# Performance work log

Measured on AMD Instinct MI355X. Metric: run time of the kernel, lower is better.

The kernel has to match this reference:

```python
import jax, jax.numpy as jnp
import numpy as np

D, H = 1536, 16
HD = D // H            # head_dim = 96
ROPE_CH = HD // 2      # rope_channels_ratio=0.5 -> RoPE on last 48 channels
FF = 4 * D             # SwiGLU hidden
EPS = 1e-6
MAX_WAVELENGTH = 10000.0


def _ln(x):
    # LayerNorm, elementwise_affine=False, eps=1e-6
    m = jnp.mean(x, axis=-1, keepdims=True)
    v = jnp.var(x, axis=-1, keepdims=True)
    return (x - m) * jax.lax.rsqrt(v + EPS)


def _rms(x, w):
    # LlamaRMSNorm: fp32 internally
    xf = x.astype(jnp.float32)
    v = jnp.mean(jnp.square(xf), axis=-1, keepdims=True)
    return (w * (xf * jax.lax.rsqrt(v + EPS))).astype(x.dtype)


def _apply_rope(q, pos):
    # q: [B,H,S,hd], pos: [B,S]
    hd = q.shape[-1]
    frac = 2.0 * jnp.arange(hd // 2, dtype=jnp.float32) / hd
    timescale = MAX_WAVELENGTH ** frac                       # [hd/2]
    sin_inp = pos.astype(jnp.float32)[:, None, :, None] / timescale  # [B,1,S,hd/2]
    sin, cos = jnp.sin(sin_inp), jnp.cos(sin_inp)
    a, b = jnp.split(q, 2, axis=-1)
    out = jnp.concatenate([a * cos - b * sin, b * cos + a * sin], axis=-1)
    return out.astype(q.dtype)


def _rotary(x, pos, ch):
    # apply RoPE to the last `ch` channels of head_dim
    left, right = x[..., :-ch], x[..., -ch:]
    return jnp.concatenate([left, _apply_rope(right, pos)], axis=-1)


def _mod(x, shift, scale):
    # t2i_modulate: x * (1 + scale) + shift, cond broadcast over seq
    return x * (1.0 + scale[:, None, :]) + shift[:, None, :]


def setup_inputs() -> dict:
    key = jax.random.key(0)
    ks = jax.random.split(key, 32)
    B, Nx, Ny = 1, 2048, 256
    w = lambda k, shp: (0.02 * jax.random.normal(k, shp, dtype=jnp.float32))
    inp = {
        'x': jax.random.normal(ks[0], (B, Nx, D), dtype=jnp.float32),
        'y': jax.random.normal(ks[1], (B, Ny, D), dtype=jnp.float32),
        't': jax.random.normal(ks[2], (B, D), dtype=jnp.float32),
        'positions': jnp.arange(Nx, dtype=jnp.int32).reshape(B, Nx),
        'w_mod_x': w(ks[3], (D, 6 * D)), 'b_mod_x': jnp.zeros((6 * D,), jnp.float32),
        'w_mod_y': w(ks[4], (D, 6 * D)), 'b_mod_y': jnp.zeros((6 * D,), jnp.float32),
        'w_qkv_x': w(ks[5], (D, 3 * D)), 'b_qkv_x': jnp.zeros((3 * D,), jnp.float32),
        'w_qkv_y': w(ks[6], (D, 3 * D)), 'b_qkv_y': jnp.zeros((3 * D,), jnp.float32),
        'qn_x': jnp.ones((HD,), jnp.float32), 'kn_x': jnp.ones((HD,), jnp.float32),
        'qn_y': jnp.ones((HD,), jnp.float32), 'kn_y': jnp.ones((HD,), jnp.float32),
        'w_proj_x': w(ks[7], (D, D)), 'b_proj_x': jnp.zeros((D,), jnp.float32),
        'w_proj_y': w(ks[8], (D, D)), 'b_proj_y': jnp.zeros((D,), jnp.float32),
        'w1_x': w(ks[9], (D, FF)), 'w2_x': w(ks[10], (D, FF)), 'w3_x': w(ks[11], (FF, D)),
        'w1_y': w(ks[12], (D, FF)), 'w2_y': w(ks[13], (D, FF)), 'w3_y': w(ks[14], (FF, D)),
    }
    return inp


def reference(x, y, t, positions,
              w_mod_x, b_mod_x, w_mod_y, b_mod_y,
              w_qkv_x, b_qkv_x, w_qkv_y, b_qkv_y,
              qn_x, kn_x, qn_y, kn_y,
              w_proj_x, b_proj_x, w_proj_y, b_proj_y,
              w1_x, w2_x, w3_x, w1_y, w2_y, w3_y):
    B, Nx, _ = x.shape
    Ny = y.shape[1]
    st = jax.nn.silu(t)
    sh1x, sc1x, g1x, sh2x, sc2x, g2x = jnp.split(st @ w_mod_x + b_mod_x, 6, axis=-1)
    sh1y, sc1y, g1y, sh2y, sc2y, g2y = jnp.split(st @ w_mod_y + b_mod_y, 6, axis=-1)

    def qkv(z, w, b, qn, kn, pos):
        q, k, v = jnp.split(z @ w + b, 3, axis=-1)
        r = lambda u: u.reshape(B, -1, H, HD).transpose(0, 2, 1, 3)  # [B,H,S,hd]
        q, k, v = r(q), r(k), r(v)
        q, k = _rms(q, qn), _rms(k, kn)
        if pos is not None:
            q, k = _rotary(q, pos, ROPE_CH), _rotary(k, pos, ROPE_CH)
        return q, k, v

    qx, kx, vx = qkv(_mod(_ln(x), sh1x, sc1x), w_qkv_x, b_qkv_x, qn_x, kn_x, positions)
    qy, ky, vy = qkv(_mod(_ln(y), sh1y, sc1y), w_qkv_y, b_qkv_y, qn_y, kn_y, None)

    q = jnp.concatenate([qx, qy], axis=2)
    k = jnp.concatenate([kx, ky], axis=2)
    v = jnp.concatenate([vx, vy], axis=2)
    scores = jnp.einsum('bhqd,bhkd->bhqk', q, k) * (HD ** -0.5)
    attn = jax.nn.softmax(scores, axis=-1)
    o = jnp.einsum('bhqk,bhkd->bhqd', attn, v)
    o = o.transpose(0, 2, 1, 3).reshape(B, Nx + Ny, D)
    ox, oy = o[:, :Nx], o[:, Nx:]

    x = x + g1x[:, None, :] * (ox @ w_proj_x + b_proj_x)
    y = y + g1y[:, None, :] * (oy @ w_proj_y + b_proj_y)

    def ffn(z, w1, w2, w3):
        return (jax.nn.silu(z @ w1) * (z @ w2)) @ w3

    x = x + g2x[:, None, :] * ffn(_mod(_ln(x), sh2x, sc2x), w1_x, w2_x, w3_x)
    y = y + g2y[:, None, :] * ffn(_mod(_ln(y), sh2y, sc2y), w1_y, w2_y, w3_y)
    return jnp.concatenate([x, y], axis=1)
```

## Files before the change

### kernel.cpp

```cpp
#include <hip/hip_runtime.h>
#include <hip/hip_bf16.h>

#define D_  1536
#define H_  16
#define HD_ 96
#define NX_ 2048
#define NY_ 256
#define NT_ 2304
#define FF_ 6144
#define EPS_ 1e-6f

typedef unsigned short u16;
typedef unsigned int   u32;
typedef short short8 __attribute__((ext_vector_type(8)));
typedef float f32x4  __attribute__((ext_vector_type(4)));
typedef unsigned short u16x4 __attribute__((ext_vector_type(4)));

__device__ __forceinline__ u16 f2bf(float f){
    u32 u = __float_as_uint(f);
    return (u16)((u + 0x7fffu + ((u >> 16) & 1u)) >> 16);
}
__device__ __forceinline__ float bf2f(u16 h){ return __uint_as_float(((u32)h) << 16); }

__device__ __forceinline__ void gll16(const void* g, void* l){
    __builtin_amdgcn_global_load_lds(
        (const __attribute__((address_space(1))) unsigned int*)g,
        (__attribute__((address_space(3))) unsigned int*)l, 16, 0, 0);
}

__global__ __launch_bounds__(256) void transpose_k(
    const float* __restrict__ Wx, const float* __restrict__ Wy,
    u16* __restrict__ Ox, u16* __restrict__ Oy, int K, int N)
{
    const float* W = blockIdx.y ? Wy : Wx;
    u16* O = blockIdx.y ? Oy : Ox;
    int tn_cnt = N >> 5;
    int tk = blockIdx.x / tn_cnt, tn = blockIdx.x % tn_cnt;
    __shared__ float tile[32][33];
    int t = threadIdx.x;
    {
        int k = t >> 3, n4 = (t & 7) * 4;
        float4 v = *(const float4*)&W[(size_t)(tk*32 + k) * N + tn*32 + n4];
        tile[k][n4+0] = v.x; tile[k][n4+1] = v.y;
        tile[k][n4+2] = v.z; tile[k][n4+3] = v.w;
    }
    __syncthreads();
    {
        int n = t >> 3, k4 = (t & 7) * 4;
        u16x4 r;
        #pragma unroll
        for (int i = 0; i < 4; i++) r[i] = f2bf(tile[k4+i][n]);
        *(u16x4*)&O[(size_t)(tn*32 + n) * K + tk*32 + k4] = r;
    }
}

__global__ __launch_bounds__(256) void modvec2_k(
    const float* __restrict__ t_in,
    const float* __restrict__ w_mod_x, const float* __restrict__ w_mod_y,
    float* __restrict__ pbuf)
{
    int part = blockIdx.y;
    int j = blockIdx.x * 256 + threadIdx.x;
    __shared__ float st[96];
    int k0 = part * 96;
    if (threadIdx.x < 96){
        float v = t_in[k0 + threadIdx.x];
        st[threadIdx.x] = v / (1.f + __expf(-v));
    }
    __syncthreads();
    const float* W; int col;
    if (j < 6*D_){ W = w_mod_x; col = j; }
    else         { W = w_mod_y; col = j - 6*D_; }
    const float* wp = W + (size_t)k0 * (6*D_) + col;
    float acc = 0.f;
    #pragma unroll 8
    for (int k = 0; k < 96; k++)
        acc += st[k] * wp[(size_t)k * (6*D_)];
    pbuf[(size_t)part * 18432 + j] = acc;
}

__global__ __launch_bounds__(256) void reducemod_k(
    const float* __restrict__ pbuf,
    const float* __restrict__ b_mod_x, const float* __restrict__ b_mod_y,
    float* __restrict__ modx, float* __restrict__ mody)
{
    int j = blockIdx.x * 256 + threadIdx.x;
    float acc = (j < 6*D_) ? b_mod_x[j] : b_mod_y[j - 6*D_];
    #pragma unroll
    for (int p = 0; p < 16; p++)
        acc += pbuf[(size_t)p * 18432 + j];
    if (j < 6*D_) modx[j] = acc;
    else          mody[j - 6*D_] = acc;
}

__global__ __launch_bounds__(256) void lnmod_k(
    const float* __restrict__ inx, const float* __restrict__ iny,
    const float* __restrict__ modx, const float* __restrict__ mody,
    int shoff, u16* __restrict__ out)
{
    int row = blockIdx.x, t = threadIdx.x;
    const float* in; const float* mod;
    if (row < NX_){ in = inx + (size_t)row * D_;        mod = modx; }
    else          { in = iny + (size_t)(row-NX_) * D_;  mod = mody; }
    const float* sh = mod + shoff;
    const float* sc = mod + shoff + D_;
    float vals[6]; float s = 0.f, ss = 0.f;
    #pragma unroll
    for (int j = 0; j < 6; j++){
        float v = in[t + j*256];
        vals[j] = v; s += v; ss += v*v;
    }
    for (int mask = 1; mask < 64; mask <<= 1){
        s  += __shfl_xor(s,  mask);
        ss += __shfl_xor(ss, mask);
    }
    __shared__ float red[2][4];
    int wave = t >> 6, lane = t & 63;
    if (lane == 0){ red[0][wave] = s; red[1][wave] = ss; }
    __syncthreads();
    s  = red[0][0] + red[0][1] + red[0][2] + red[0][3];
    ss = red[1][0] + red[1][1] + red[1][2] + red[1][3];
    float mean = s * (1.f / D_);
    float var  = ss * (1.f / D_) - mean * mean;
    float inv  = rsqrtf(var + EPS_);
    #pragma unroll
    for (int j = 0; j < 6; j++){
        int c = t + j*256;
        float z = (vals[j] - mean) * inv;
        z = z * (1.f + sc[c]) + sh[c];
        out[(size_t)row * D_ + c] = f2bf(z);
    }
}

template<int MODE>
__global__ __launch_bounds__(512, 2) void gemm3_k(
    const u16* __restrict__ A,
    const u16* __restrict__ BTx, const u16* __restrict__ BTy,
    const float* __restrict__ biasx, const float* __restrict__ biasy,
    const u16* __restrict__ hmul,
    u16* __restrict__ outB, int ldo,
    int K, int mb, int nb)
{
    __shared__ u16 As[2][256*64];
    __shared__ u16 Bs[2][256*64];
    int nwg = mb * nb;
    int bid = blockIdx.x;
    int q = nwg >> 3, r = nwg & 7, xcd = bid & 7;
    int wgid = (xcd < r ? xcd*(q+1) : r*(q+1) + (xcd - r)*q) + (bid >> 3);
    int bm = wgid % mb, bn = wgid / mb;
    int sel = (bm == mb - 1);
    int row0 = bm * 256, col0 = bn * 256;
    const u16* Bt = sel ? BTy : BTx;

    int t = threadIdx.x, wid = t >> 6, lane = t & 63;
    int lrow = lane & 15, lgrp = lane >> 4;
    int wr = (wid >> 2) * 128, wc = (wid & 3) * 64;

    const char* Ab = (const char*)(A  + (size_t)row0 * K);
    const char* Bb = (const char*)(Bt + (size_t)col0 * K);
    u32 offG[4], offL[4];
    #pragma unroll
    for (int i = 0; i < 4; i++){
        int rr = i*64 + (t >> 3);
        int cc = (t & 7) ^ (rr & 7);
        offG[i] = (u32)(rr * K + cc * 8) * 2;
        offL[i] = (u32)(i*8192 + t*16);
    }

    #define STAGEG(bsel, kb) do{                                                  \
        _Pragma("unroll")                                                         \
        for (int i = 0; i < 4; i++)                                               \
            gll16(Ab + (offG[i] + (kb)), (char*)As[bsel] + offL[i]);              \
        _Pragma("unroll")                                                         \
        for (int i = 0; i < 4; i++)                                               \
            gll16(Bb + (offG[i] + (kb)), (char*)Bs[bsel] + offL[i]);              \
    } while(0)

    f32x4 acc[8][4];
    #pragma unroll
    for (int i = 0; i < 8; i++)
        #pragma unroll
        for (int j = 0; j < 4; j++) acc[i][j] = (f32x4){0.f,0.f,0.f,0.f};

    int nt = K >> 6;
    STAGEG(0, 0);

    for (int tt = 0; tt < nt; tt++){
        const u16* Ac = As[tt & 1];
        const u16* Bc = Bs[tt & 1];
        if (tt + 1 < nt){
            STAGEG((tt + 1) & 1, (u32)(tt + 1) * 128);
            asm volatile("s_waitcnt vmcnt(8)" ::: "memory");
        } else {
            asm volatile("s_waitcnt vmcnt(0)" ::: "memory");
        }
        __builtin_amdgcn_sched_barrier(0);
        __builtin_amdgcn_s_barrier();
        __builtin_amdgcn_sched_barrier(0);
        #pragma unroll
        for (int kk = 0; kk < 2; kk++){
            int pc = ((kk*4 + lgrp) ^ (lrow & 7)) * 8;
            short8 bf[4];
            #pragma unroll
            for (int ni = 0; ni < 4; ni++)
                bf[ni] = *(const short8*)&Bc[(wc + ni*16 + lrow)*64 + pc];
            #pragma unroll
            for (int mi = 0; mi < 8; mi++){
                short8 af = *(const short8*)&Ac[(wr + mi*16 + lrow)*64 + pc];
                #pragma unroll
                for (int ni = 0; ni < 4; ni++)
                    acc[mi][ni] = __builtin_amdgcn_mfma_f32_16x16x32_bf16(
                                      af, bf[ni], acc[mi][ni], 0, 0, 0);
            }
        }
        asm volatile("s_waitcnt lgkmcnt(0)" ::: "memory");
        __builtin_amdgcn_sched_barrier(0);
        __builtin_amdgcn_s_barrier();
        __builtin_amdgcn_sched_barrier(0);
    }
    #undef STAGEG

    const float* biasp = sel ? biasy : biasx;
    #pragma unroll
    for (int mi = 0; mi < 8; mi++){
        #pragma unroll
        for (int ni = 0; ni < 4; ni++){
            #pragma unroll
            for (int rr = 0; rr < 4; rr++){
                int gr = row0 + wr + mi*16 + lgrp*4 + rr;
                int gc = col0 + wc + ni*16 + lrow;
                float v = acc[mi][ni][rr];
                size_t oi = (size_t)gr * ldo + gc;
                if (MODE == 0)      outB[oi] = f2bf(v + biasp[gc]);
                else if (MODE == 2) outB[oi] = f2bf(v / (1.f + __expf(-v)));
                else if (MODE == 3) outB[oi] = f2bf(bf2f(hmul[oi]) * v);
            }
        }
    }
}

template<int MODE>
__global__ __launch_bounds__(256, 2) void gemm2_k(
    const u16* __restrict__ A, int lda,
    const u16* __restrict__ BTx, const u16* __restrict__ BTy, int ldb,
    const float* __restrict__ biasx, const float* __restrict__ biasy,
    const float* __restrict__ residx, const float* __restrict__ residy,
    const float* __restrict__ gmodx, const float* __restrict__ gmody,
    float* __restrict__ outF, int ldo,
    int K, int nb, int kparts)
{
    __shared__ u16 As[2][128*64];
    __shared__ u16 Bs[2][128*64];
    int nwg_base = 18 * nb;
    int nwg = nwg_base * kparts;
    int bid = blockIdx.x;
    int bid2 = (bid & 7) * (nwg >> 3) + (bid >> 3);
    int ks  = bid2 / nwg_base;
    int rem = bid2 % nwg_base;
    int bm = rem % 18, bn = rem / 18;
    int sel = (bm >= 16);
    int row0 = bm * 128, col0 = bn * 128;
    const u16* Bt = (sel ? BTy : BTx) + (size_t)ks * K;
    const u16* Ap = A + (size_t)ks * K;
    outF += (size_t)ks * NT_ * D_;

    int t = threadIdx.x, w = t >> 6, l = t & 63;
    int lrow = l & 15, lgrp = l >> 4;
    int wr = (w >> 1) * 64, wc = (w & 1) * 64;

    const char* Ab = (const char*)(Ap + (size_t)row0 * lda);
    const char* Bb = (const char*)(Bt + (size_t)col0 * ldb);
    u32 offA[4], offB[4], ldsoff[4];
    #pragma unroll
    for (int i = 0; i < 4; i++){
        int r = (i*4 + w)*8 + (l >> 3);
        int c = (l & 7) ^ (r & 7);
        offA[i]   = (u32)(r * lda + c * 8) * 2;
        offB[i]   = (u32)(r * ldb + c * 8) * 2;
        ldsoff[i] = (u32)((i*4 + w) * 1024);
    }

    #define STAGEG(bsel, kb) do{                                                  \
        _Pragma("unroll")                                                         \
        for (int i = 0; i < 4; i++)                                               \
            gll16(Ab + (offA[i] + (kb)), (char*)As + (bsel)*16384 + ldsoff[i]);   \
        _Pragma("unroll")                                                         \
        for (int i = 0; i < 4; i++)                                               \
            gll16(Bb + (offB[i] + (kb)), (char*)Bs + (bsel)*16384 + ldsoff[i]);   \
    } while(0)

    f32x4 acc[4][4];
    #pragma unroll
    for (int i = 0; i < 4; i++)
        #pragma unroll
        for (int j = 0; j < 4; j++) acc[i][j] = (f32x4){0.f,0.f,0.f,0.f};

    int nt = K >> 6;
    STAGEG(0, 0);

    for (int tt = 0; tt < nt; tt++){
        const u16* Ac = As[tt & 1];
        const u16* Bc = Bs[tt & 1];
        if (tt + 1 < nt){
            STAGEG((tt + 1) & 1, (u32)(tt + 1) * 128);
            asm volatile("s_waitcnt vmcnt(8)" ::: "memory");
        } else {
            asm volatile("s_waitcnt vmcnt(0)" ::: "memory");
        }
        __builtin_amdgcn_sched_barrier(0);
        __builtin_amdgcn_s_barrier();
        __builtin_amdgcn_sched_barrier(0);
        #pragma unroll
        for (int kk = 0; kk < 2; kk++){
            int pc = ((kk*4 + lgrp) ^ (lrow & 7)) * 8;
            short8 af[4], bf[4];
            #pragma unroll
            for (int mi = 0; mi < 4; mi++)
                af[mi] = *(const short8*)&Ac[(wr + mi*16 + lrow)*64 + pc];
            #pragma unroll
            for (int ni = 0; ni < 4; ni++)
                bf[ni] = *(const short8*)&Bc[(wc + ni*16 + lrow)*64 + pc];
            #pragma unroll
            for (int mi = 0; mi < 4; mi++)
                #pragma unroll
                for (int ni = 0; ni < 4; ni++)
                    acc[mi][ni] = __builtin_amdgcn_mfma_f32_16x16x32_bf16(
                                      af[mi], bf[ni], acc[mi][ni], 0, 0, 0);
        }
        asm volatile("s_waitcnt lgkmcnt(0)" ::: "memory");
        __builtin_amdgcn_sched_barrier(0);
        __builtin_amdgcn_s_barrier();
        __builtin_amdgcn_sched_barrier(0);
    }
    #undef STAGEG

    const float* biasp  = sel ? biasy  : biasx;
    const float* residp = sel ? residy : residx;
    const float* gmodp  = sel ? gmody  : gmodx;
    #pragma unroll
    for (int mi = 0; mi < 4; mi++){
        #pragma unroll
        for (int ni = 0; ni < 4; ni++){
            #pragma unroll
            for (int r = 0; r < 4; r++){
                int gr = row0 + wr + mi*16 + lgrp*4 + r;
                int gc = col0 + wc + ni*16 + lrow;
                float v = acc[mi][ni][r];
                size_t oi = (size_t)gr * ldo + gc;
                if (MODE == 1)      outF[oi] = residp[oi] + gmodp[gc] * (v + biasp[gc]);
                else if (MODE == 5) outF[oi] = v;
            }
        }
    }
}

__global__ __launch_bounds__(256) void reduce_k(
    const float* __restrict__ p, const float* __restrict__ x1,
    const float* __restrict__ modx, const float* __restrict__ mody,
    float* __restrict__ dout)
{
    size_t i = ((size_t)blockIdx.x * 256 + threadIdx.x) * 4;
    float4 a = *(const float4*)&p[i];
    float4 b = *(const float4*)&p[(size_t)NT_ * D_ + i];
    float4 r = *(const float4*)&x1[i];
    int row = (int)(i / D_), col = (int)(i % D_);
    const float* g = (row < NX_ ? modx : mody) + 5*D_;
    float4 gv = *(const float4*)&g[col];
    float4 o;
    o.x = r.x + gv.x * (a.x + b.x);
    o.y = r.y + gv.y * (a.y + b.y);
    o.z = r.z + gv.z * (a.z + b.z);
    o.w = r.w + gv.w * (a.w + b.w);
    *(float4*)&dout[i] = o;
}

__global__ __launch_bounds__(256) void qkvpost_k(
    const u16* __restrict__ qkvraw, const int* __restrict__ positions,
    const float* __restrict__ qn_x, const float* __restrict__ kn_x,
    const float* __restrict__ qn_y, const float* __restrict__ kn_y,
    u16* __restrict__ Qg, u16* __restrict__ Kg, u16* __restrict__ Vg)
{
    int tok = blockIdx.x;
    int t = threadIdx.x, wave = t >> 6, lane = t & 63;
    bool isx = tok < NX_;
    float pos = isx ? (float)positions[tok] : 0.f;
    const float* qn = isx ? qn_x : qn_y;
    const float* kn = isx ? kn_x : kn_y;
    bool act = lane < 48;
    int d = lane * 2;
    #pragma unroll
    for (int hh = 0; hh < 4; hh++){
        int h = wave + hh * 4;
        const u16* base = qkvraw + (size_t)tok * (3*D_) + h * HD_;
        float qx=0.f,qy=0.f,kx=0.f,ky=0.f,vx=0.f,vy=0.f;
        if (act){
            u32 qw = *(const u32*)(base + d);
            u32 kw = *(const u32*)(base + D_ + d);
            u32 vw = *(const u32*)(base + 2*D_ + d);
            qx = bf2f((u16)qw); qy = bf2f((u16)(qw >> 16));
            kx = bf2f((u16)kw); ky = bf2f((u16)(kw >> 16));
            vx = bf2f((u16)vw); vy = bf2f((u16)(vw >> 16));
        }
        float sq = qx*qx + qy*qy, sk = kx*kx + ky*ky;
        for (int mask = 1; mask < 64; mask <<= 1){
            sq += __shfl_xor(sq, mask);
            sk += __shfl_xor(sk, mask);
        }
        float rq = rsqrtf(sq / (float)HD_ + EPS_);
        float rk = rsqrtf(sk / (float)HD_ + EPS_);
        if (act){
            qx *= rq * qn[d]; qy *= rq * qn[d+1];
            kx *= rk * kn[d]; ky *= rk * kn[d+1];
        }
        int pl = (lane < 36) ? lane + 12 : lane - 12;
        float qpx = __shfl(qx, pl), qpy = __shfl(qy, pl);
        float kpx = __shfl(kx, pl), kpy = __shfl(ky, pl);
        if (isx && lane >= 24 && act){
            bool aside = lane < 36;
            int i0 = aside ? (2*lane - 48) : (2*lane - 72);
            float ang0 = pos * __powf(10000.f, -(float)i0 / 24.f);
            float ang1 = pos * __powf(10000.f, -(float)(i0+1) / 24.f);
            float s0,c0,s1,c1;
            __sincosf(ang0, &s0, &c0);
            __sincosf(ang1, &s1, &c1);
            if (aside){
                qx = qx*c0 - qpx*s0;  qy = qy*c1 - qpy*s1;
                kx = kx*c0 - kpx*s0;  ky = ky*c1 - kpy*s1;
            } else {
                qx = qx*c0 + qpx*s0;  qy = qy*c1 + qpy*s1;
                kx = kx*c0 + kpx*s0;  ky = ky*c1 + kpy*s1;
            }
        }
        size_t o96  = ((size_t)h * NT_ + tok) * 96;
        size_t o128 = ((size_t)h * NT_ + tok) * 128;
        if (act){
            Qg[o96 + d] = f2bf(qx);  Qg[o96 + d + 1] = f2bf(qy);
            Kg[o128 + d] = f2bf(kx); Kg[o128 + d + 1] = f2bf(ky);
            Vg[o96 + d] = f2bf(vx);  Vg[o96 + d + 1] = f2bf(vy);
        } else {
            int dp = 96 + (lane - 48) * 2;
            Kg[o128 + dp] = 0; Kg[o128 + dp + 1] = 0;
        }
    }
}

__global__ __launch_bounds__(256) void vtrans_k(
    const u16* __restrict__ Vg, u16* __restrict__ Vtg)
{
    int h = blockIdx.y, t0 = blockIdx.x * 64;
    __shared__ u16 tile[64][104];
    int t = threadIdx.x;
    #pragma unroll
    for (int i = 0; i < 3; i++){
        int idx = i*256 + t;
        int tok = idx / 12, c = idx % 12;
        uint4 v = *(const uint4*)&Vg[((size_t)h*NT_ + t0 + tok)*96 + c*8];
        *(uint4*)&tile[tok][c*8] = v;
    }
    __syncthreads();
    #pragma unroll
    for (int i = 0; i < 3; i++){
        int idx = i*256 + t;
        int d = idx >> 3, tc = idx & 7;
        u16 vv[8];
        #pragma unroll
        for (int j = 0; j < 8; j++) vv[j] = tile[tc*8 + j][d];
        *(uint4*)&Vtg[((size_t)h*128 + d)*NT_ + t0 + tc*8] = *(uint4*)vv;
    }
    {
        int row = 96 + (t >> 3), tc = t & 7;
        u16 val = (row == 96) ? (u16)0x3F80 : (u16)0;
        u16 vv[8];
        #pragma unroll
        for (int j = 0; j < 8; j++) vv[j] = val;
        *(uint4*)&Vtg[((size_t)h*128 + row)*NT_ + t0 + tc*8] = *(uint4*)vv;
    }
}

__global__ __launch_bounds__(256, 4) void attn_k(
    const u16* __restrict__ Qg, const u16* __restrict__ Kg,
    const u16* __restrict__ Vtg, u16* __restrict__ Og)
{
    int bid = blockIdx.x;
    int bid2 = (bid & 7) * 72 + (bid >> 3);
    int h = bid2 / 36;
    int q0 = (bid2 % 36) * 64;
    __shared__ u16 Ks[64*128];
    __shared__ u16 Vs[112*64];
    __shared__ u16 Ps[4][16*72];
    int t = threadIdx.x, wave = t >> 6, lane = t & 63;
    int lrow = lane & 15, lgrp = lane >> 4;
    const float C1 = (float)(0.10206207261596577 * 1.4426950408889634);
    const float C2 = (float)(-10.0 * 1.4426950408889634);

    const u16* qbase = Qg + ((size_t)h * NT_ + q0 + wave*16 + lrow) * 96;
    short8 qf[3];
    #pragma unroll
    for (int c = 0; c < 3; c++) qf[c] = *(const short8*)(qbase + c*32 + lgrp*8);

    const u16* Kbh = Kg  + (size_t)h * NT_ * 128;
    const u16* Vbh = Vtg + (size_t)h * 128 * NT_;

    int krow[4], kc_[4], vrow[4], vc_[4];
    #pragma unroll
    for (int i = 0; i < 4; i++){
        int g = wave*4 + i;
        krow[i] = g*4 + (lane >> 4);
        kc_[i]  = (lane & 15) ^ (krow[i] & 7);
        vrow[i] = g*8 + (lane >> 3);
        vc_[i]  = (lane & 7) ^ (vrow[i] & 7);
    }

    f32x4 oacc[7];
    #pragma unroll
    for (int n = 0; n < 7; n++) oacc[n] = (f32x4){0.f,0.f,0.f,0.f};

    for (int kt = 0; kt < NT_/64; kt++){
        __syncthreads();
        #pragma unroll
        for (int i = 0; i < 4; i++)
            gll16(Kbh + ((size_t)(kt*64 + krow[i]))*128 + kc_[i]*8,
                  &Ks[(wave*4 + i)*512 + lane*8]);
        #pragma unroll
        for (int i = 0; i < 4; i++){
            int g = wave*4 + i;
            if (g < 14)
                gll16(Vbh + (size_t)vrow[i]*NT_ + kt*64 + vc_[i]*8,
                      &Vs[g*512 + lane*8]);
        }
        __syncthreads();

        f32x4 s[4];
        #pragma unroll
        for (int nt = 0; nt < 4; nt++){
            s[nt] = (f32x4){0.f,0.f,0.f,0.f};
            #pragma unroll
            for (int c = 0; c < 3; c++){
                int pc = ((c*4 + lgrp) ^ (lrow & 7)) * 8;
                short8 kf = *(const short8*)&Ks[(nt*16 + lrow)*128 + pc];
                s[nt] = __builtin_amdgcn_mfma_f32_16x16x32_bf16(kf, qf[c], s[nt], 0,0,0);
            }
        }
        #pragma unroll
        for (int nt = 0; nt < 4; nt++){
            u32 lo = (u32)f2bf(exp2f(fmaf(s[nt][0], C1, C2)))
                   | ((u32)f2bf(exp2f(fmaf(s[nt][1], C1, C2))) << 16);
            u32 hi = (u32)f2bf(exp2f(fmaf(s[nt][2], C1, C2)))
                   | ((u32)f2bf(exp2f(fmaf(s[nt][3], C1, C2))) << 16);
            uint2 pk; pk.x = lo; pk.y = hi;
            *(uint2*)&Ps[wave][lrow*72 + nt*16 + lgrp*4] = pk;
        }
        #pragma unroll
        for (int kc = 0; kc < 2; kc++){
            short8 pf = *(const short8*)&Ps[wave][lrow*72 + kc*32 + lgrp*8];
            #pragma unroll
            for (int n = 0; n < 7; n++){
                int pc = ((kc*4 + lgrp) ^ (lrow & 7)) * 8;
                short8 vf = *(const short8*)&Vs[(n*16 + lrow)*64 + pc];
                oacc[n] = __builtin_amdgcn_mfma_f32_16x16x32_bf16(pf, vf, oacc[n], 0,0,0);
            }
        }
    }

    float linv[4];
    #pragma unroll
    for (int r = 0; r < 4; r++)
        linv[r] = 1.f / __shfl(oacc[6][r], lane & 48);

    #pragma unroll
    for (int n = 0; n < 6; n++){
        #pragma unroll
        for (int r = 0; r < 4; r++){
            int tok = q0 + wave*16 + lgrp*4 + r;
            Og[(size_t)tok * D_ + h*HD_ + n*16 + lrow] = f2bf(oacc[n][r] * linv[r]);
        }
    }
}

extern "C" void kernel_launch(void* const* d_in, const int* in_sizes, int n_in,
                              void* d_out, int out_size, void* d_ws, size_t ws_size,
                              hipStream_t stream)
{
    const float* x        = (const float*)d_in[0];
    const float* y        = (const float*)d_in[1];
    const float* tt       = (const float*)d_in[2];
    const int*   pos      = (const int*)  d_in[3];
    const float* w_mod_x  = (const float*)d_in[4];
    const float* b_mod_x  = (const float*)d_in[5];
    const float* w_mod_y  = (const float*)d_in[6];
    const float* b_mod_y  = (const float*)d_in[7];
    const float* w_qkv_x  = (const float*)d_in[8];
    const float* b_qkv_x  = (const float*)d_in[9];
    const float* w_qkv_y  = (const float*)d_in[10];
    const float* b_qkv_y  = (const float*)d_in[11];
    const float* qn_x     = (const float*)d_in[12];
    const float* kn_x     = (const float*)d_in[13];
    const float* qn_y     = (const float*)d_in[14];
    const float* kn_y     = (const float*)d_in[15];
    const float* w_proj_x = (const float*)d_in[16];
    const float* b_proj_x = (const float*)d_in[17];
    const float* w_proj_y = (const float*)d_in[18];
    const float* b_proj_y = (const float*)d_in[19];
    const float* w1_x     = (const float*)d_in[20];
    const float* w2_x     = (const float*)d_in[21];
    const float* w3_x     = (const float*)d_in[22];
    const float* w1_y     = (const float*)d_in[23];
    const float* w2_y     = (const float*)d_in[24];
    const float* w3_y     = (const float*)d_in[25];
    float* dout = (float*)d_out;

    char* ws = (char*)d_ws;
    size_t off = 0;
    float* modx   = (float*)(ws + off); off += (size_t)(6*D_) * 4;
    float* mody   = (float*)(ws + off); off += (size_t)(6*D_) * 4;
    u16*   a      = (u16*)  (ws + off); off += (size_t)NT_ * D_ * 2;
    u16*   arena  = (u16*)  (ws + off); off += (size_t)2 * D_ * FF_ * 2;
    u16*   r1     = (u16*)  (ws + off); off += (size_t)NT_ * FF_ * 2;
    u16*   r2     = (u16*)  (ws + off); off += ((size_t)3*96 + 128) * H_ * NT_ * 2;
    float* x1     = (float*)(ws + off); off += (size_t)NT_ * D_ * 4;
    u16*   Vtg    = (u16*)  (ws + off); off += (size_t)H_ * 128 * NT_ * 2;

    float* pmod   = (float*)arena;
    u16*   qkvraw = r1;
    u16*   hs     = r1;
    float* p0     = (float*)r1;
    u16*   Qb     = r2;
    u16*   Kb     = r2 + (size_t)H_ * NT_ * 96;
    u16*   Vb     = r2 + (size_t)H_ * NT_ * (96 + 128);
    u16*   Ob     = r2 + (size_t)H_ * NT_ * (2*96 + 128);
    u16*   hb     = r2;

    const size_t qkvW  = (size_t)D_ * (3*D_);
    const size_t projW = (size_t)D_ * D_;
    const size_t ffW   = (size_t)D_ * FF_;

    modvec2_k<<<dim3(72, 16), 256, 0, stream>>>(tt, w_mod_x, w_mod_y, pmod);
    reducemod_k<<<72, 256, 0, stream>>>(pmod, b_mod_x, b_mod_y, modx, mody);
    lnmod_k<<<NT_, 256, 0, stream>>>(x, y, modx, mody, 0, a);
    transpose_k<<<dim3(48*144, 2), 256, 0, stream>>>(w_qkv_x, w_qkv_y, arena, arena + qkvW, D_, 3*D_);
    gemm3_k<0><<<9*18, 512, 0, stream>>>(a, arena, arena + qkvW, b_qkv_x, b_qkv_y,
        nullptr, qkvraw, 3*D_, D_, 9, 18);
    qkvpost_k<<<NT_, 256, 0, stream>>>(qkvraw, pos, qn_x, kn_x, qn_y, kn_y, Qb, Kb, Vb);
    vtrans_k<<<dim3(36, 16), 256, 0, stream>>>(Vb, Vtg);
    attn_k<<<576, 256, 0, stream>>>(Qb, Kb, Vtg, Ob);
    transpose_k<<<dim3(48*48, 2), 256, 0, stream>>>(w_proj_x, w_proj_y, arena, arena + projW, D_, D_);
    gemm2_k<1><<<18*12, 256, 0, stream>>>(Ob, D_, arena, arena + projW, D_,
        b_proj_x, b_proj_y, x, y - (size_t)NX_*D_, modx + 2*D_, mody + 2*D_,
        x1, D_, D_, 12, 1);
    lnmod_k<<<NT_, 256, 0, stream>>>(x1, x1 + (size_t)NX_*D_, modx, mody, 3*D_, a);
    transpose_k<<<dim3(48*192, 2), 256, 0, stream>>>(w1_x, w1_y, arena, arena + ffW, D_, FF_);
    gemm3_k<2><<<9*24, 512, 0, stream>>>(a, arena, arena + ffW, nullptr, nullptr,
        nullptr, hs, FF_, D_, 9, 24);
    transpose_k<<<dim3(48*192, 2), 256, 0, stream>>>(w2_x, w2_y, arena, arena + ffW, D_, FF_);
    gemm3_k<3><<<9*24, 512, 0, stream>>>(a, arena, arena + ffW, nullptr, nullptr,
        hs, hb, FF_, D_, 9, 24);
    transpose_k<<<dim3(192*48, 2), 256, 0, stream>>>(w3_x, w3_y, arena, arena + ffW, FF_, D_);
    gemm2_k<5><<<18*12*2, 256, 0, stream>>>(hb, FF_, arena, arena + ffW, FF_,
        nullptr, nullptr, nullptr, nullptr, nullptr, nullptr,
        p0, D_, 3072, 12, 2);
    reduce_k<<<(NT_*D_/4)/256, 256, 0, stream>>>(p0, x1, modx, mody, dout);
    (void)in_sizes; (void)n_in; (void)out_size; (void)ws_size;
}
```

Before: 491.0 us.

## Load K fragments directly into registers with prefetch, drop K LDS staging

The attention kernel no longer stages K tiles through shared memory. Each lane loads its K MFMA fragments straight from global memory into registers, and the next tile is prefetched during the current tile's compute. K is stored unpadded at head dimension 96 instead of 128, so the workspace layout and the qkvpost writes change to match. This cuts LDS traffic and K bytes read, but adds many registers (24 short8), so the launch-bounds occupancy hint drops from 4 to 3 blocks and the global reads are no longer coalesced through LDS.

```diff
diff --git a/kernel.cpp b/kernel.cpp
--- a/kernel.cpp
+++ b/kernel.cpp
@@ -431,15 +431,11 @@
                 kx = kx*c0 + kpx*s0;  ky = ky*c1 + kpy*s1;
             }
         }
-        size_t o96  = ((size_t)h * NT_ + tok) * 96;
-        size_t o128 = ((size_t)h * NT_ + tok) * 128;
         if (act){
-            Qg[o96 + d] = f2bf(qx);  Qg[o96 + d + 1] = f2bf(qy);
-            Kg[o128 + d] = f2bf(kx); Kg[o128 + d + 1] = f2bf(ky);
-            Vg[o96 + d] = f2bf(vx);  Vg[o96 + d + 1] = f2bf(vy);
-        } else {
-            int dp = 96 + (lane - 48) * 2;
-            Kg[o128 + dp] = 0; Kg[o128 + dp + 1] = 0;
+            size_t o = ((size_t)h * NT_ + tok) * 96 + d;
+            Qg[o] = f2bf(qx); Qg[o+1] = f2bf(qy);
+            Kg[o] = f2bf(kx); Kg[o+1] = f2bf(ky);
+            Vg[o] = f2bf(vx); Vg[o+1] = f2bf(vy);
         }
     }
 }
@@ -477,7 +473,7 @@
     }
 }
 
-__global__ __launch_bounds__(256, 4) void attn_k(
+__global__ __launch_bounds__(256, 3) void attn_k(
     const u16* __restrict__ Qg, const u16* __restrict__ Kg,
     const u16* __restrict__ Vtg, u16* __restrict__ Og)
 {
@@ -485,7 +481,6 @@
     int bid2 = (bid & 7) * 72 + (bid >> 3);
     int h = bid2 / 36;
     int q0 = (bid2 % 36) * 64;
-    __shared__ u16 Ks[64*128];
     __shared__ u16 Vs[112*64];
     __shared__ u16 Ps[4][16*72];
     int t = threadIdx.x, wave = t >> 6, lane = t & 63;
@@ -498,29 +493,31 @@
     #pragma unroll
     for (int c = 0; c < 3; c++) qf[c] = *(const short8*)(qbase + c*32 + lgrp*8);
 
-    const u16* Kbh = Kg  + (size_t)h * NT_ * 128;
+    const u16* Kbh = Kg  + (size_t)h * NT_ * 96;
     const u16* Vbh = Vtg + (size_t)h * 128 * NT_;
 
-    int krow[4], kc_[4], vrow[4], vc_[4];
+    int vrow[4], vc_[4];
     #pragma unroll
     for (int i = 0; i < 4; i++){
         int g = wave*4 + i;
-        krow[i] = g*4 + (lane >> 4);
-        kc_[i]  = (lane & 15) ^ (krow[i] & 7);
         vrow[i] = g*8 + (lane >> 3);
         vc_[i]  = (lane & 7) ^ (vrow[i] & 7);
     }
+    const u16* kfp = Kbh + (size_t)(lrow) * 96 + lgrp*8;
 
     f32x4 oacc[7];
     #pragma unroll
     for (int n = 0; n < 7; n++) oacc[n] = (f32x4){0.f,0.f,0.f,0.f};
+
+    short8 kc[12], kn[12];
+    #pragma unroll
+    for (int nt = 0; nt < 4; nt++)
+        #pragma unroll
+        for (int c = 0; c < 3; c++)
+            kc[nt*3 + c] = *(const short8*)(kfp + (size_t)(nt*16)*96 + c*32);
 
     for (int kt = 0; kt < NT_/64; kt++){
         __syncthreads();
-        #pragma unroll
-        for (int i = 0; i < 4; i++)
-            gll16(Kbh + ((size_t)(kt*64 + krow[i]))*128 + kc_[i]*8,
-                  &Ks[(wave*4 + i)*512 + lane*8]);
         #pragma unroll
         for (int i = 0; i < 4; i++){
             int g = wave*4 + i;
@@ -530,16 +527,22 @@
         }
         __syncthreads();
 
+        if (kt + 1 < NT_/64){
+            const u16* kfn = kfp + (size_t)(kt + 1) * 64 * 96;
+            #pragma unroll
+            for (int nt = 0; nt < 4; nt++)
+                #pragma unroll
+                for (int c = 0; c < 3; c++)
+                    kn[nt*3 + c] = *(const short8*)(kfn + (size_t)(nt*16)*96 + c*32);
+        }
+
         f32x4 s[4];
         #pragma unroll
         for (int nt = 0; nt < 4; nt++){
             s[nt] = (f32x4){0.f,0.f,0.f,0.f};
             #pragma unroll
-            for (int c = 0; c < 3; c++){
-                int pc = ((c*4 + lgrp) ^ (lrow & 7)) * 8;
-                short8 kf = *(const short8*)&Ks[(nt*16 + lrow)*128 + pc];
-                s[nt] = __builtin_amdgcn_mfma_f32_16x16x32_bf16(kf, qf[c], s[nt], 0,0,0);
-            }
+            for (int c = 0; c < 3; c++)
+                s[nt] = __builtin_amdgcn_mfma_f32_16x16x32_bf16(kc[nt*3 + c], qf[c], s[nt], 0,0,0);
         }
         #pragma unroll
         for (int nt = 0; nt < 4; nt++){
@@ -551,14 +554,18 @@
             *(uint2*)&Ps[wave][lrow*72 + nt*16 + lgrp*4] = pk;
         }
         #pragma unroll
-        for (int kc = 0; kc < 2; kc++){
-            short8 pf = *(const short8*)&Ps[wave][lrow*72 + kc*32 + lgrp*8];
+        for (int kc2 = 0; kc2 < 2; kc2++){
+            short8 pf = *(const short8*)&Ps[wave][lrow*72 + kc2*32 + lgrp*8];
             #pragma unroll
             for (int n = 0; n < 7; n++){
-                int pc = ((kc*4 + lgrp) ^ (lrow & 7)) * 8;
+                int pc = ((kc2*4 + lgrp) ^ (lrow & 7)) * 8;
                 short8 vf = *(const short8*)&Vs[(n*16 + lrow)*64 + pc];
                 oacc[n] = __builtin_amdgcn_mfma_f32_16x16x32_bf16(pf, vf, oacc[n], 0,0,0);
             }
+        }
+        if (kt + 1 < NT_/64){
+            #pragma unroll
+            for (int i = 0; i < 12; i++) kc[i] = kn[i];
         }
     }
 
@@ -616,7 +623,7 @@
     u16*   a      = (u16*)  (ws + off); off += (size_t)NT_ * D_ * 2;
     u16*   arena  = (u16*)  (ws + off); off += (size_t)2 * D_ * FF_ * 2;
     u16*   r1     = (u16*)  (ws + off); off += (size_t)NT_ * FF_ * 2;
-    u16*   r2     = (u16*)  (ws + off); off += ((size_t)3*96 + 128) * H_ * NT_ * 2;
+    u16*   r2     = (u16*)  (ws + off); off += (size_t)4 * 96 * H_ * NT_ * 2;
     float* x1     = (float*)(ws + off); off += (size_t)NT_ * D_ * 4;
     u16*   Vtg    = (u16*)  (ws + off); off += (size_t)H_ * 128 * NT_ * 2;
 
@@ -626,8 +633,8 @@
     float* p0     = (float*)r1;
     u16*   Qb     = r2;
     u16*   Kb     = r2 + (size_t)H_ * NT_ * 96;
-    u16*   Vb     = r2 + (size_t)H_ * NT_ * (96 + 128);
-    u16*   Ob     = r2 + (size_t)H_ * NT_ * (2*96 + 128);
+    u16*   Vb     = r2 + (size_t)2 * H_ * NT_ * 96;
+    u16*   Ob     = r2 + (size_t)3 * H_ * NT_ * 96;
     u16*   hb     = r2;
 
     const size_t qkvW  = (size_t)D_ * (3*D_);
```

New measurement: 520.1 us. 5.9% more time.

## Split attention KV range across two blocks and combine partials in separate kernel

Applied to the files above, without the earlier changes.

Each attention block now processes half of the key/value tiles and writes unnormalized fp32 output accumulators plus the row-sum column to a scratch buffer; a new combine kernel adds the two halves and normalizes. This doubles the number of attention blocks to better fill the GPU's compute units. It adds fp32 partial write/read traffic and an extra kernel launch, and relies on the fixed-offset exponent so partials can be summed directly.

```diff
diff --git a/kernel.cpp b/kernel.cpp
--- a/kernel.cpp
+++ b/kernel.cpp
@@ -479,10 +479,12 @@
 
 __global__ __launch_bounds__(256, 4) void attn_k(
     const u16* __restrict__ Qg, const u16* __restrict__ Kg,
-    const u16* __restrict__ Vtg, u16* __restrict__ Og)
+    const u16* __restrict__ Vtg, float* __restrict__ pbuf)
 {
     int bid = blockIdx.x;
-    int bid2 = (bid & 7) * 72 + (bid >> 3);
+    int kvh = (bid >= 576);
+    int bb  = bid - kvh * 576;
+    int bid2 = (bb & 7) * 72 + (bb >> 3);
     int h = bid2 / 36;
     int q0 = (bid2 % 36) * 64;
     __shared__ u16 Ks[64*128];
@@ -515,7 +517,8 @@
     #pragma unroll
     for (int n = 0; n < 7; n++) oacc[n] = (f32x4){0.f,0.f,0.f,0.f};
 
-    for (int kt = 0; kt < NT_/64; kt++){
+    int kt0 = kvh * 18;
+    for (int kt = kt0; kt < kt0 + 18; kt++){
         __syncthreads();
         #pragma unroll
         for (int i = 0; i < 4; i++)
@@ -551,29 +554,40 @@
             *(uint2*)&Ps[wave][lrow*72 + nt*16 + lgrp*4] = pk;
         }
         #pragma unroll
-        for (int kc = 0; kc < 2; kc++){
-            short8 pf = *(const short8*)&Ps[wave][lrow*72 + kc*32 + lgrp*8];
+        for (int kc2 = 0; kc2 < 2; kc2++){
+            short8 pf = *(const short8*)&Ps[wave][lrow*72 + kc2*32 + lgrp*8];
             #pragma unroll
             for (int n = 0; n < 7; n++){
-                int pc = ((kc*4 + lgrp) ^ (lrow & 7)) * 8;
+                int pc = ((kc2*4 + lgrp) ^ (lrow & 7)) * 8;
                 short8 vf = *(const short8*)&Vs[(n*16 + lrow)*64 + pc];
                 oacc[n] = __builtin_amdgcn_mfma_f32_16x16x32_bf16(pf, vf, oacc[n], 0,0,0);
             }
         }
     }
 
-    float linv[4];
-    #pragma unroll
-    for (int r = 0; r < 4; r++)
-        linv[r] = 1.f / __shfl(oacc[6][r], lane & 48);
-
-    #pragma unroll
-    for (int n = 0; n < 6; n++){
+    float* pb = pbuf + ((size_t)(bid2*2 + kvh)) * (64*112);
+    #pragma unroll
+    for (int n = 0; n < 7; n++){
         #pragma unroll
         for (int r = 0; r < 4; r++){
-            int tok = q0 + wave*16 + lgrp*4 + r;
-            Og[(size_t)tok * D_ + h*HD_ + n*16 + lrow] = f2bf(oacc[n][r] * linv[r]);
-        }
+            int row = wave*16 + lgrp*4 + r;
+            pb[(size_t)row * 112 + n*16 + lrow] = oacc[n][r];
+        }
+    }
+}
+
+__global__ __launch_bounds__(256) void attncomb_k(
+    const float* __restrict__ pbuf, u16* __restrict__ Og)
+{
+    int cid = blockIdx.x;
+    int h = cid / 36, q0 = (cid % 36) * 64;
+    const float* p0 = pbuf + ((size_t)(cid*2 + 0)) * (64*112);
+    const float* p1 = pbuf + ((size_t)(cid*2 + 1)) * (64*112);
+    for (int e = threadIdx.x; e < 64*96; e += 256){
+        int row = e / 96, col = e % 96;
+        float l = p0[row*112 + 96] + p1[row*112 + 96];
+        float o = (p0[row*112 + col] + p1[row*112 + col]) / l;
+        Og[(size_t)(q0 + row) * D_ + h*HD_ + col] = f2bf(o);
     }
 }
 
@@ -621,6 +635,7 @@
     u16*   Vtg    = (u16*)  (ws + off); off += (size_t)H_ * 128 * NT_ * 2;
 
     float* pmod   = (float*)arena;
+    float* attnp  = (float*)arena;
     u16*   qkvraw = r1;
     u16*   hs     = r1;
     float* p0     = (float*)r1;
@@ -642,7 +657,8 @@
         nullptr, qkvraw, 3*D_, D_, 9, 18);
     qkvpost_k<<<NT_, 256, 0, stream>>>(qkvraw, pos, qn_x, kn_x, qn_y, kn_y, Qb, Kb, Vb);
     vtrans_k<<<dim3(36, 16), 256, 0, stream>>>(Vb, Vtg);
-    attn_k<<<576, 256, 0, stream>>>(Qb, Kb, Vtg, Ob);
+    attn_k<<<1152, 256, 0, stream>>>(Qb, Kb, Vtg, attnp);
+    attncomb_k<<<576, 256, 0, stream>>>(attnp, Ob);
     transpose_k<<<dim3(48*48, 2), 256, 0, stream>>>(w_proj_x, w_proj_y, arena, arena + projW, D_, D_);
     gemm2_k<1><<<18*12, 256, 0, stream>>>(Ob, D_, arena, arena + projW, D_,
         b_proj_x, b_proj_y, x, y - (size_t)NX_*D_, modx + 2*D_, mody + 2*D_,
```

New measurement: 489.6 us. No clear change (-0.3%).
